# Performance work log

Measured on AMD Instinct MI355X. Metric: run time of the kernel, lower is better.

Reference implementation:

```python
import jax, jax.numpy as jnp
import numpy as np

N_QUBITS = 10   # log2(32*32)
N_LAYERS = 5
GRID = 32


def _u3_gates(weights):
    # weights: [L, Q, 3] float32 -> gates: [L, Q, 2, 2] complex64
    th, ph, lm = weights[..., 0], weights[..., 1], weights[..., 2]
    cos = jnp.cos(th / 2)
    sin = jnp.sin(th / 2)
    u00 = cos.astype(jnp.complex64)
    u01 = -jnp.exp(1j * lm) * sin
    u10 = jnp.exp(1j * ph) * sin
    u11 = jnp.exp(1j * (ph + lm)) * cos
    row0 = jnp.stack([u00, u01], axis=-1)
    row1 = jnp.stack([u10, u11], axis=-1)
    return jnp.stack([row0, row1], axis=-2)


def _build_unitary(weights):
    N = 1 << N_QUBITS
    gates = _u3_gates(weights)
    # U as tensor [N, 2, 2, ..., 2]; axis q+1 is qubit q's column index
    U = jnp.eye(N, dtype=jnp.complex64).reshape((N,) + (2,) * N_QUBITS)
    for l in range(N_LAYERS):
        # single-qubit U3 rotations
        for q in range(N_QUBITS):
            ax = q + 1
            s = jnp.moveaxis(U, ax, -1)
            s = jnp.einsum('...a,ba->...b', s, gates[l, q])
            U = jnp.moveaxis(s, -1, ax)
        # circular CNOTs: control q -> target (q+1) % N_QUBITS
        for q in range(N_QUBITS):
            c_ax = q + 1
            t_ax = ((q + 1) % N_QUBITS) + 1
            s = jnp.moveaxis(U, (c_ax, t_ax), (-2, -1))
            # when control bit == 1, flip target bit (swap the two target slices)
            s = s.at[..., 1, :].set(s[..., 1, ::-1])
            U = jnp.moveaxis(s, (-2, -1), (c_ax, t_ax))
    return U.reshape(N, N)


def setup_inputs() -> dict:
    key = jax.random.key(0)
    k1, k2 = jax.random.split(key)
    x_freq = jax.random.normal(k1, (128, 16, GRID, GRID), dtype=jnp.float32)
    weights = jax.random.normal(k2, (N_LAYERS, N_QUBITS, 3), dtype=jnp.float32) * 0.1
    return {"x_freq": x_freq, "weights": weights}


def reference(x_freq, weights):
    B, C, H, W = x_freq.shape
    state = x_freq.reshape(B, C, -1).astype(jnp.complex64)  # [B, C, N]
    U = _build_unitary(weights)                              # [N, N]
    out = jnp.einsum('ij,bcj->bci', U, state)
    return out.reshape(B, C, H, W)
```

## Files before the change

kernel.cpp:

```cpp
#include <hip/hip_runtime.h>


#define NQ 10
#define NL 5
#define NST 1024
#define NTH 256

constexpr int csigma(int i) {
  for (int q = 0; q < NQ; ++q) {
    const int cb = 9 - q;
    const int tb = 9 - ((q + 1) % NQ);
    i ^= ((i >> cb) & 1) << tb;
  }
  return i;
}

__device__ __forceinline__ int swz(int k) { return k ^ (((k >> 4) & 3) << 2); }

__global__ void build_gates(const float* __restrict__ w, float* __restrict__ gw) {
  const int t = threadIdx.x;
  if (t < NL * NQ) {
    const float th = w[t * 3 + 0], ph = w[t * 3 + 1], lm = w[t * 3 + 2];
    const float ch = cosf(0.5f * th), sh = sinf(0.5f * th);
    const float cl = cosf(lm), sl = sinf(lm);
    const float cp = cosf(ph), sp = sinf(ph);
    const float cpl = cosf(ph + lm), spl = sinf(ph + lm);
    float* G = gw + t * 8;
    G[0] = ch;       G[1] = 0.0f;
    G[2] = cp * sh;  G[3] = sp * sh;
    G[4] = -cl * sh; G[5] = -sl * sh;
    G[6] = cpl * ch; G[7] = spl * ch;
  }
}

__device__ __forceinline__ void bfly(float2& a, float2& b,
                                     const float4 g0, const float4 g1) {
  const float nar = g0.x * a.x - g0.y * a.y + g0.z * b.x - g0.w * b.y;
  const float nai = g0.x * a.y + g0.y * a.x + g0.z * b.y + g0.w * b.x;
  const float nbr = g1.x * a.x - g1.y * a.y + g1.z * b.x - g1.w * b.y;
  const float nbi = g1.x * a.y + g1.y * a.x + g1.z * b.y + g1.w * b.x;
  a = make_float2(nar, nai);
  b = make_float2(nbr, nbi);
}

__global__ __launch_bounds__(NTH, 8) void qc_apply(
    const float* __restrict__ x, const float* __restrict__ gw,
    float* __restrict__ out, int out_size) {
  __shared__ float2 sc[NST];
  const int s = blockIdx.x, t = threadIdx.x;

  const float4 xv = ((const float4*)(x + (size_t)s * NST))[t];
  {
    const int p0 = swz(4 * t);
    float4* s4 = (float4*)sc;
    s4[p0 / 2]     = make_float4(xv.x, 0.f, xv.y, 0.f);
    s4[p0 / 2 + 1] = make_float4(xv.z, 0.f, xv.w, 0.f);
  }
  __syncthreads();

  constexpr int S1 = csigma(1 << 8);
  constexpr int S2 = csigma(1 << 9);

  for (int l = NL - 1; l >= 0; --l) {
    const float4* g = (const float4*)(gw + (size_t)l * NQ * 8);

    {
      int sb = t;
#pragma unroll
      for (int q = 0; q < NQ; ++q) {
        const int cb = 9 - q, tb = 9 - ((q + 1) % NQ);
        sb ^= ((sb >> cb) & 1) << tb;
      }
      float2 v00 = sc[swz(sb)];
      float2 v01 = sc[swz(sb ^ S1)];
      float2 v10 = sc[swz(sb ^ S2)];
      float2 v11 = sc[swz(sb ^ S1 ^ S2)];
      const float4 h1a = g[2], h1b = g[3];
      const float4 h2a = g[0], h2b = g[1];
      bfly(v00, v01, h1a, h1b);
      bfly(v10, v11, h1a, h1b);
      bfly(v00, v10, h2a, h2b);
      bfly(v01, v11, h2a, h2b);
      __syncthreads();
      sc[swz(t)]       = v00;
      sc[swz(t + 256)] = v01;
      sc[swz(t + 512)] = v10;
      sc[swz(t + 768)] = v11;
      __syncthreads();
    }

#pragma unroll
    for (int p = 3; p >= 0; --p) {
      const int b1 = 2 * p;
      const int m1 = 1 << b1;
      const int base = ((t >> b1) << (b1 + 2)) | (t & (m1 - 1));
      float2 v00 = sc[swz(base)];
      float2 v01 = sc[swz(base + m1)];
      float2 v10 = sc[swz(base + 2 * m1)];
      float2 v11 = sc[swz(base + 3 * m1)];
      const int q1 = 9 - b1;
      const float4 h1a = g[2 * q1],     h1b = g[2 * q1 + 1];
      const float4 h2a = g[2 * q1 - 2], h2b = g[2 * q1 - 1];
      bfly(v00, v01, h1a, h1b);
      bfly(v10, v11, h1a, h1b);
      bfly(v00, v10, h2a, h2b);
      bfly(v01, v11, h2a, h2b);
      sc[swz(base)]          = v00;
      sc[swz(base + m1)]     = v01;
      sc[swz(base + 2 * m1)] = v10;
      sc[swz(base + 3 * m1)] = v11;
      __syncthreads();
    }
  }

  const size_t ob = (size_t)s * NST;
#pragma unroll
  for (int j = 0; j < 4; ++j) {
    const int k = t + j * NTH;
    if (ob + (size_t)k < (size_t)out_size) out[ob + k] = sc[swz(k)].x;
  }
}

extern "C" void kernel_launch(void* const* d_in, const int* in_sizes, int n_in,
                              void* d_out, int out_size, void* d_ws, size_t ws_size,
                              hipStream_t stream) {
  const float* x = (const float*)d_in[0];
  const float* w = (const float*)d_in[1];
  float* out = (float*)d_out;
  float* gw = (float*)d_ws;
  const int nstates = in_sizes[0] / NST;
  build_gates<<<1, 64, 0, stream>>>(w, gw);
  qc_apply<<<nstates, NTH, 0, stream>>>(x, gw, out, out_size);
}
```

Measured before the change: 93.34 us.

## Register-resident 5-qubit blocks with 32 lanes per statevector

Rewrites the kernel so each 32-lane half of a 64-thread block owns one 1024-amplitude state and holds 32 amplitudes per thread in registers. Each layer is applied as two 5-qubit passes with a single shared-memory transpose between them, replacing the previous 2-qubit passes that each went through shared memory. The CNOT permutation is folded into the gather indices, the swizzle is changed to suit the new access pattern, and the final pass writes output straight from registers as float4. The aims are fewer LDS round trips and barriers, at the cost of heavy register use, lower occupancy, and 32-lane halves on a 64-wide wavefront.

```diff
diff --git a/kernel.cpp b/kernel.cpp
--- a/kernel.cpp
+++ b/kernel.cpp
@@ -4,18 +4,18 @@
 #define NQ 10
 #define NL 5
 #define NST 1024
-#define NTH 256
+#define NTH 64
+#define SV_STRIDE 1028
 
 constexpr int csigma(int i) {
   for (int q = 0; q < NQ; ++q) {
-    const int cb = 9 - q;
-    const int tb = 9 - ((q + 1) % NQ);
+    const int cb = 9 - q, tb = 9 - ((q + 1) % NQ);
     i ^= ((i >> cb) & 1) << tb;
   }
   return i;
 }
 
-__device__ __forceinline__ int swz(int k) { return k ^ (((k >> 4) & 3) << 2); }
+__device__ __forceinline__ int swz(int k) { return k ^ (((k >> 5) & 15) << 1); }
 
 __global__ void build_gates(const float* __restrict__ w, float* __restrict__ gw) {
   const int t = threadIdx.x;
@@ -33,91 +33,117 @@
   }
 }
 
-__device__ __forceinline__ void bfly(float2& a, float2& b,
-                                     const float4 g0, const float4 g1) {
-  const float nar = g0.x * a.x - g0.y * a.y + g0.z * b.x - g0.w * b.y;
-  const float nai = g0.x * a.y + g0.y * a.x + g0.z * b.y + g0.w * b.x;
-  const float nbr = g1.x * a.x - g1.y * a.y + g1.z * b.x - g1.w * b.y;
-  const float nbi = g1.x * a.y + g1.y * a.x + g1.z * b.y + g1.w * b.x;
+__device__ __forceinline__ void bfly(float2& a, float2& b, const float h00,
+                                     const float2 h01, const float2 h10,
+                                     const float2 h11) {
+  const float nar = h00 * a.x + h01.x * b.x - h01.y * b.y;
+  const float nai = h00 * a.y + h01.x * b.y + h01.y * b.x;
+  const float nbr = h10.x * a.x - h10.y * a.y + h11.x * b.x - h11.y * b.y;
+  const float nbi = h10.x * a.y + h10.y * a.x + h11.x * b.y + h11.y * b.x;
   a = make_float2(nar, nai);
   b = make_float2(nbr, nbi);
 }
 
-__global__ __launch_bounds__(NTH, 8) void qc_apply(
+__global__ __launch_bounds__(NTH) void qc_apply(
     const float* __restrict__ x, const float* __restrict__ gw,
     float* __restrict__ out, int out_size) {
-  __shared__ float2 sc[NST];
-  const int s = blockIdx.x, t = threadIdx.x;
+  __shared__ float2 sc[2 * SV_STRIDE];
 
-  const float4 xv = ((const float4*)(x + (size_t)s * NST))[t];
+  const int t = threadIdx.x;
+  const int lane = t & 31;
+  const int svLocal = t >> 5;
+  const int svGlobal = blockIdx.x * 2 + svLocal;
+  const int svo = svLocal * SV_STRIDE;
+  float4* const s4 = (float4*)(sc + svo);
+
   {
-    const int p0 = swz(4 * t);
-    float4* s4 = (float4*)sc;
-    s4[p0 / 2]     = make_float4(xv.x, 0.f, xv.y, 0.f);
-    s4[p0 / 2 + 1] = make_float4(xv.z, 0.f, xv.w, 0.f);
+    const float* xs = x + (size_t)svGlobal * NST;
+#pragma unroll
+    for (int r = 0; r < 8; ++r) {
+      const int k = lane * 4 + 128 * r;
+      const float4 xv = *(const float4*)(xs + k);
+      const int p01 = swz(k);
+      const int p23 = p01 ^ 2;
+      *(float4*)&sc[svo + p01] = make_float4(xv.x, 0.f, xv.y, 0.f);
+      *(float4*)&sc[svo + p23] = make_float4(xv.z, 0.f, xv.w, 0.f);
+    }
   }
   __syncthreads();
 
-  constexpr int S1 = csigma(1 << 8);
-  constexpr int S2 = csigma(1 << 9);
+  int sL = lane;
+#pragma unroll
+  for (int q = 0; q < NQ; ++q) {
+    const int cb = 9 - q, tb = 9 - ((q + 1) % NQ);
+    sL ^= ((sL >> cb) & 1) << tb;
+  }
+  constexpr int SH0 = csigma(1 << 5), SH1 = csigma(1 << 6),
+                SH2 = csigma(1 << 7), SH3 = csigma(1 << 8),
+                SH4 = csigma(1 << 9);
 
+  const int m = (lane & 15) << 1;
+  float2 w2[32];
+
+#pragma unroll 1
   for (int l = NL - 1; l >= 0; --l) {
-    const float4* g = (const float4*)(gw + (size_t)l * NQ * 8);
+    const float* gl = gw + l * NQ * 8;
 
-    {
-      int sb = t;
+    float2 v[32];
 #pragma unroll
-      for (int q = 0; q < NQ; ++q) {
-        const int cb = 9 - q, tb = 9 - ((q + 1) % NQ);
-        sb ^= ((sb >> cb) & 1) << tb;
-      }
-      float2 v00 = sc[swz(sb)];
-      float2 v01 = sc[swz(sb ^ S1)];
-      float2 v10 = sc[swz(sb ^ S2)];
-      float2 v11 = sc[swz(sb ^ S1 ^ S2)];
-      const float4 h1a = g[2], h1b = g[3];
-      const float4 h2a = g[0], h2b = g[1];
-      bfly(v00, v01, h1a, h1b);
-      bfly(v10, v11, h1a, h1b);
-      bfly(v00, v10, h2a, h2b);
-      bfly(v01, v11, h2a, h2b);
-      __syncthreads();
-      sc[swz(t)]       = v00;
-      sc[swz(t + 256)] = v01;
-      sc[swz(t + 512)] = v10;
-      sc[swz(t + 768)] = v11;
-      __syncthreads();
+    for (int j = 0; j < 32; ++j) {
+      const int idx = sL ^ ((j & 1) ? SH0 : 0) ^ ((j & 2) ? SH1 : 0) ^
+                      ((j & 4) ? SH2 : 0) ^ ((j & 8) ? SH3 : 0) ^
+                      ((j & 16) ? SH4 : 0);
+      v[j] = sc[svo + swz(idx)];
     }
+#pragma unroll
+    for (int e = 0; e < 5; ++e) {
+      const float* G = gl + (4 - e) * 8;
+      const float h00 = G[0];
+      const float2 h01 = make_float2(G[2], G[3]);
+      const float2 h10 = make_float2(G[4], G[5]);
+      const float2 h11 = make_float2(G[6], G[7]);
+#pragma unroll
+      for (int j = 0; j < 32; ++j)
+        if (!(j & (1 << e))) bfly(v[j], v[j | (1 << e)], h00, h01, h10, h11);
+    }
+    __syncthreads();
+#pragma unroll
+    for (int j = 0; j < 32; ++j)
+      sc[svo + swz((j << 5) | lane)] = v[j];
+    __syncthreads();
 
 #pragma unroll
-    for (int p = 3; p >= 0; --p) {
-      const int b1 = 2 * p;
-      const int m1 = 1 << b1;
-      const int base = ((t >> b1) << (b1 + 2)) | (t & (m1 - 1));
-      float2 v00 = sc[swz(base)];
-      float2 v01 = sc[swz(base + m1)];
-      float2 v10 = sc[swz(base + 2 * m1)];
-      float2 v11 = sc[swz(base + 3 * m1)];
-      const int q1 = 9 - b1;
-      const float4 h1a = g[2 * q1],     h1b = g[2 * q1 + 1];
-      const float4 h2a = g[2 * q1 - 2], h2b = g[2 * q1 - 1];
-      bfly(v00, v01, h1a, h1b);
-      bfly(v10, v11, h1a, h1b);
-      bfly(v00, v10, h2a, h2b);
-      bfly(v01, v11, h2a, h2b);
-      sc[swz(base)]          = v00;
-      sc[swz(base + m1)]     = v01;
-      sc[swz(base + 2 * m1)] = v10;
-      sc[swz(base + 3 * m1)] = v11;
+    for (int a = 0; a < 16; ++a) {
+      const float4 p = s4[((lane << 5) + ((2 * a) ^ m)) >> 1];
+      w2[2 * a]     = make_float2(p.x, p.y);
+      w2[2 * a + 1] = make_float2(p.z, p.w);
+    }
+#pragma unroll
+    for (int e = 0; e < 5; ++e) {
+      const float* G = gl + (9 - e) * 8;
+      const float h00 = G[0];
+      const float2 h01 = make_float2(G[2], G[3]);
+      const float2 h10 = make_float2(G[4], G[5]);
+      const float2 h11 = make_float2(G[6], G[7]);
+#pragma unroll
+      for (int i = 0; i < 32; ++i)
+        if (!(i & (1 << e))) bfly(w2[i], w2[i | (1 << e)], h00, h01, h10, h11);
+    }
+    if (l != 0) {
+#pragma unroll
+      for (int a = 0; a < 16; ++a)
+        s4[((lane << 5) + ((2 * a) ^ m)) >> 1] =
+            make_float4(w2[2 * a].x, w2[2 * a].y, w2[2 * a + 1].x, w2[2 * a + 1].y);
       __syncthreads();
     }
   }
 
-  const size_t ob = (size_t)s * NST;
+  const size_t ob = (size_t)svGlobal * NST + (lane << 5);
 #pragma unroll
-  for (int j = 0; j < 4; ++j) {
-    const int k = t + j * NTH;
-    if (ob + (size_t)k < (size_t)out_size) out[ob + k] = sc[swz(k)].x;
+  for (int a = 0; a < 8; ++a) {
+    if (ob + 4 * a + 4 <= (size_t)out_size)
+      *(float4*)(out + ob + 4 * a) =
+          make_float4(w2[4 * a].x, w2[4 * a + 1].x, w2[4 * a + 2].x, w2[4 * a + 3].x);
   }
 }
 
@@ -130,5 +156,5 @@
   float* gw = (float*)d_ws;
   const int nstates = in_sizes[0] / NST;
   build_gates<<<1, 64, 0, stream>>>(w, gw);
-  qc_apply<<<nstates, NTH, 0, stream>>>(x, gw, out, out_size);
+  qc_apply<<<nstates / 2, NTH, 0, stream>>>(x, gw, out, out_size);
 }
```

Result: no change. 93.52 us (+0.2%).
